# Kernel tuning notes

Measured on AMD Instinct MI355X. Metric: run time of the kernel, lower is better.

## Reference

```python
import jax, jax.numpy as jnp
import numpy as np

B, N, C = 16, 4096, 91            # images, proposals/image, classes (incl. background)
H, W = 800.0, 1333.0              # image shape
SCORE_THRESH = 0.05
NMS_THRESH = 0.5
K = 100                           # detections_per_img (greedy NMS steps)
M = 4096                          # top-M candidate prefilter before NMS
OFFSET = 1.0e4                    # class offset for batched NMS (>> max coord)
DW_CLAMP = float(np.log(1000.0 / 16.0))


def setup_inputs():
    key = jax.random.key(0)
    k1, k2, k3, k4, k5, k6 = jax.random.split(key, 6)
    class_logits = jax.random.normal(k1, (B * N, C), jnp.float32) * 2.0
    box_regression = jax.random.normal(k2, (B * N, C * 4), jnp.float32) * 0.1
    # valid proposal boxes (x1 < x2, y1 < y2, inside image)
    x1 = jax.random.uniform(k3, (B, N, 1)) * (W - 64.0)
    y1 = jax.random.uniform(k4, (B, N, 1)) * (H - 64.0)
    bw = jax.random.uniform(k5, (B, N, 1)) * 256.0 + 16.0
    bh = jax.random.uniform(k6, (B, N, 1)) * 256.0 + 16.0
    proposals = jnp.concatenate([x1, y1, jnp.minimum(x1 + bw, W), jnp.minimum(y1 + bh, H)], -1)
    return {"class_logits": class_logits, "box_regression": box_regression, "proposals": proposals}


def _decode_and_clip(rel, props):
    w = props[..., 2] - props[..., 0]
    h = props[..., 3] - props[..., 1]
    cx = props[..., 0] + 0.5 * w
    cy = props[..., 1] + 0.5 * h
    dx = rel[..., 0] / 10.0
    dy = rel[..., 1] / 10.0
    dw = jnp.minimum(rel[..., 2] / 5.0, DW_CLAMP)
    dh = jnp.minimum(rel[..., 3] / 5.0, DW_CLAMP)
    pcx = dx * w[..., None] + cx[..., None]
    pcy = dy * h[..., None] + cy[..., None]
    pw = jnp.exp(dw) * w[..., None]
    ph = jnp.exp(dh) * h[..., None]
    boxes = jnp.stack([
        jnp.clip(pcx - 0.5 * pw, 0.0, W),
        jnp.clip(pcy - 0.5 * ph, 0.0, H),
        jnp.clip(pcx + 0.5 * pw, 0.0, W),
        jnp.clip(pcy + 0.5 * ph, 0.0, H)], -1)  # [B,N,C,4]
    return boxes


def _greedy_nms(boxes, scores):
    # boxes: [M,4] (already class-offset), scores: [M] (suppressed entries == -1)
    x1, y1, x2, y2 = boxes[:, 0], boxes[:, 1], boxes[:, 2], boxes[:, 3]
    area = (x2 - x1) * (y2 - y1)

    def step(sc, _):
        i = jnp.argmax(sc)
        s = sc[i]
        valid = s > 0.0
        iw = jnp.clip(jnp.minimum(x2, x2[i]) - jnp.maximum(x1, x1[i]), 0.0)
        ih = jnp.clip(jnp.minimum(y2, y2[i]) - jnp.maximum(y1, y1[i]), 0.0)
        inter = iw * ih
        iou = inter / (area + area[i] - inter + 1e-9)
        sc = jnp.where((iou > NMS_THRESH) & valid, -1.0, sc)
        sc = sc.at[i].set(-1.0)
        return sc, (i, s, valid)

    _, (idx, ss, vv) = jax.lax.scan(step, scores, None, length=K)
    return idx, ss, vv


def _post_image(boxes_all, scores_all):
    # boxes_all: [N,C,4] decoded+clipped, scores_all: [N,C] softmax scores
    boxes = boxes_all[:, 1:, :].reshape(-1, 4)          # drop background class 0
    scores = scores_all[:, 1:].reshape(-1)              # [N*(C-1)], class fastest
    labels = jnp.tile(jnp.arange(1, C, dtype=jnp.int32), N)
    scores = jnp.where(scores > SCORE_THRESH, scores, -1.0)
    top_s, top_i = jax.lax.top_k(scores, M)
    b = boxes[top_i]
    l = labels[top_i]
    ob = b + (l.astype(jnp.float32) * OFFSET)[:, None]  # batched_nms class-offset trick
    idx, ss, vv = _greedy_nms(ob, top_s)
    out_boxes = jnp.where(vv[:, None], b[idx], 0.0)     # [K,4]
    out_scores = jnp.where(vv, ss, 0.0)                 # [K]
    out_labels = jnp.where(vv, l[idx], -1)              # [K]
    return out_boxes, out_scores, out_labels, vv


def reference(class_logits, box_regression, proposals):
    pred_scores = jax.nn.softmax(class_logits, -1).reshape(B, N, C)
    rel = box_regression.reshape(B, N, C, 4)
    pred_boxes = _decode_and_clip(rel, proposals)
    boxes, scores, labels, valid = jax.vmap(_post_image)(pred_boxes, pred_scores)
    return boxes, scores, labels, valid
```

## Files before the change

kernel.cpp:

```cpp
#include <hip/hip_runtime.h>

typedef unsigned long long u64;
typedef unsigned int u32;

#define BDIM 16
#define NP   4096
#define NC   91
#define NCM1 90
#define MSEL 4096
#define NSORT 1024
#define KOUT 100
#define RSLOT 19
#define CAP_D (NP * RSLOT)
#define SCORE_T 0.05f
#define NMS_T   0.5f
#define OFFSETF 10000.0f
#define DW_CLAMP_F 4.135166556742356f
#define WF 1333.0f
#define HF 800.0f
#define GTMIN 384
#define HCAP 4096
#define FKEY (((u64)0x3E800000u) << 32)

#define TN 1024
#define RPB 64

#define DECODE_BODY(kvar, bvar, BOXDST, PACKDST)                                   \
    {                                                                              \
        int flat = (int)(~(u32)(kvar));                                            \
        int nidx = flat / NCM1;                                                    \
        int c    = flat - nidx * NCM1 + 1;                                         \
        const float* pr = props + ((long)(bvar) * NP + nidx) * 4;                  \
        float x1 = pr[0], y1 = pr[1], x2 = pr[2], y2 = pr[3];                      \
        float w = x2 - x1, h = y2 - y1;                                            \
        float cx = x1 + 0.5f * w, cy = y1 + 0.5f * h;                              \
        const float* rr = boxreg + (((long)(bvar) * NP + nidx) * NC + c) * 4;      \
        float dx = rr[0] / 10.0f, dy = rr[1] / 10.0f;                              \
        float dw = fminf(rr[2] / 5.0f, DW_CLAMP_F);                                \
        float dh = fminf(rr[3] / 5.0f, DW_CLAMP_F);                                \
        float pcx = __fadd_rn(__fmul_rn(dx, w), cx);                               \
        float pcy = __fadd_rn(__fmul_rn(dy, h), cy);                               \
        float pw  = __fmul_rn(expf(dw), w);                                        \
        float ph2 = __fmul_rn(expf(dh), h);                                        \
        float bx1 = fminf(fmaxf(pcx - 0.5f * pw, 0.0f), WF);                       \
        float by1 = fminf(fmaxf(pcy - 0.5f * ph2, 0.0f), HF);                      \
        float bx2 = fminf(fmaxf(pcx + 0.5f * pw, 0.0f), WF);                       \
        float by2 = fminf(fmaxf(pcy + 0.5f * ph2, 0.0f), HF);                      \
        BOXDST = make_float4(bx1, by1, bx2, by2);                                  \
        float offB = (float)c * OFFSETF;                                           \
        float ox1 = bx1 + offB, oy1 = by1 + offB;                                  \
        float ox2 = bx2 + offB, oy2 = by2 + offB;                                  \
        PACKDST = make_float2((ox2 - ox1) * (oy2 - oy1), (float)c);                \
    }

__global__ __launch_bounds__(1024) void k_zero(int* __restrict__ gcount,
                                               int* __restrict__ hcnt,
                                               int* __restrict__ ghist) {
    int blk = blockIdx.x;
    if (blk == 0) {
        if (threadIdx.x < BDIM) gcount[threadIdx.x] = 0;
        if (threadIdx.x >= 64 && threadIdx.x < 64 + BDIM) hcnt[threadIdx.x - 64] = 0;
    } else {
        int* g = ghist + (blk - 1) * 2048;
        for (int i = threadIdx.x; i < 2048; i += 1024) g[i] = 0;
    }
}

__global__ __launch_bounds__(256) void k_soft(const float* __restrict__ logits,
                                              u64* __restrict__ dense,
                                              int* __restrict__ gcount,
                                              u64* __restrict__ hot,
                                              int* __restrict__ hcnt,
                                              int* __restrict__ ghist) {
    __shared__ u64 stage[RPB * RSLOT];
    __shared__ u64 hstage[256];
    __shared__ int lhist[2048];
    __shared__ int s_cnt, s_base, s_hcnt, s_hbase;

    int blk  = blockIdx.x;
    int b    = blk >> 6;
    int lane = threadIdx.x & 63;
    int wid  = threadIdx.x >> 6;

    if (threadIdx.x == 0) { s_cnt = 0; s_hcnt = 0; }
    for (int i = threadIdx.x; i < 2048; i += 256) lhist[i] = 0;
    __syncthreads();

    u64 lm = (1ull << lane) - 1ull;
    for (int it = 0; it < RPB / 4; ++it) {
        int row = blk * RPB + it * 4 + wid;
        const float* lg = logits + (long)row * NC;

        float v0 = lg[lane];
        float v1 = (lane < NC - 64) ? lg[64 + lane] : -3.0e38f;
        float mx = fmaxf(v0, v1);
#pragma unroll
        for (int s = 32; s; s >>= 1) mx = fmaxf(mx, __shfl_xor(mx, s));
        float e0 = expf(v0 - mx);
        float e1 = (lane < NC - 64) ? expf(v1 - mx) : 0.0f;
        float sum = e0 + e1;
#pragma unroll
        for (int s = 32; s; s >>= 1) sum += __shfl_xor(sum, s);

        float s0 = e0 / sum;
        float s1 = e1 / sum;

        int n = row & (NP - 1);
        bool p0 = (lane >= 1) && (s0 > SCORE_T);
        bool p1 = (lane < NC - 64) && (s1 > SCORE_T);
        u64 key0 = ((u64)__float_as_uint(s0) << 32) | (u32)(~(u32)(n * NCM1 + (lane - 1)));
        u64 key1 = ((u64)__float_as_uint(s1) << 32) | (u32)(~(u32)(n * NCM1 + (64 + lane - 1)));
        u64 m0 = __ballot(p0);
        u64 m1 = __ballot(p1);
        int c0  = __popcll(m0);
        int cnt = c0 + __popcll(m1);

        int base = 0;
        if (lane == 0 && cnt) base = atomicAdd(&s_cnt, cnt);
        base = __shfl(base, 0);
        if (p0) {
            stage[base + __popcll(m0 & lm)] = key0;
            atomicAdd(&lhist[(int)(key0 >> 53)], 1);
        }
        if (p1) {
            stage[base + c0 + __popcll(m1 & lm)] = key1;
            atomicAdd(&lhist[(int)(key1 >> 53)], 1);
        }

        bool q0 = p0 && (s0 >= 0.25f);
        bool q1 = p1 && (s1 >= 0.25f);
        u64 h0 = __ballot(q0);
        u64 h1 = __ballot(q1);
        int hc0 = __popcll(h0);
        int hrow = hc0 + __popcll(h1);
        int hb = 0;
        if (lane == 0 && hrow) hb = atomicAdd(&s_hcnt, hrow);
        hb = __shfl(hb, 0);
        if (q0) hstage[hb + __popcll(h0 & lm)] = key0;
        if (q1) hstage[hb + hc0 + __popcll(h1 & lm)] = key1;
    }
    __syncthreads();

    if (threadIdx.x == 0) {
        s_base  = atomicAdd(&gcount[b], s_cnt);
        s_hbase = atomicAdd(&hcnt[b], s_hcnt);
    }
    __syncthreads();
    int m = s_cnt, base = s_base;
    u64* kb = dense + (long)b * CAP_D + base;
    for (int i = threadIdx.x; i < m; i += 256) kb[i] = stage[i];
    int hm = s_hcnt, hb2 = s_hbase;
    u64* hbp = hot + (long)b * HCAP;
    for (int i = threadIdx.x; i < hm; i += 256) {
        int pos = hb2 + i;
        if (pos < HCAP) hbp[pos] = hstage[i];
    }
    for (int i = threadIdx.x; i < 2048; i += 256) {
        int v = lhist[i];
        if (v) atomicAdd(&ghist[b * 2048 + i], v);
    }
}

__device__ __forceinline__ u64 radix_rank(const u64* __restrict__ kb, int n, int rank,
                                          int* hist, int* p_sel, int* p_gt, int tid) {
    u64 prefix = 0, mask = 0;
    const int shifts[6] = {53, 42, 31, 20, 10, 0};
    const int bitsv [6] = {11, 11, 11, 11, 10, 10};

    for (int pass = 0; pass < 6; ++pass) {
        int shift = shifts[pass];
        int nb = 1 << bitsv[pass];
        if (tid < nb) hist[tid] = 0;
        if (tid + 1024 < nb) hist[tid + 1024] = 0;
        __syncthreads();
        for (int i = tid; i < n; i += 1024) {
            u64 k = kb[i];
            if ((k & mask) == prefix)
                atomicAdd(&hist[(int)((k >> shift) & (u64)(nb - 1))], 1);
        }
        __syncthreads();
        for (int d = 1; d < nb; d <<= 1) {
            int v0 = 0, v1 = 0;
            if (tid < nb && tid + d < nb) v0 = hist[tid + d];
            if (tid + 1024 < nb && tid + 1024 + d < nb) v1 = hist[tid + 1024 + d];
            __syncthreads();
            if (tid < nb) hist[tid] += v0;
            if (tid + 1024 < nb) hist[tid + 1024] += v1;
            __syncthreads();
        }
        for (int j = tid; j < nb; j += 1024) {
            int c  = hist[j];
            int cn = (j + 1 < nb) ? hist[j + 1] : 0;
            if (c >= rank && cn < rank) { *p_sel = j; *p_gt = cn; }
        }
        __syncthreads();
        prefix |= ((u64)(*p_sel)) << shift;
        mask   |= ((u64)(nb - 1)) << shift;
        rank   -= *p_gt;
        __syncthreads();
    }
    return prefix;
}

__device__ __forceinline__ u64 radix_upper(const u64* __restrict__ kb, int n, int rank,
                                           int* hist, int* p_sel, int* p_gt, int tid) {
    int rank0 = rank;
    u64 prefix = 0, mask = 0;
    const int shifts[6] = {53, 42, 31, 20, 10, 0};
    const int bitsv [6] = {11, 11, 11, 11, 10, 10};

    for (int pass = 0; pass < 6; ++pass) {
        int shift = shifts[pass];
        int nb = 1 << bitsv[pass];
        if (tid < nb) hist[tid] = 0;
        if (tid + 1024 < nb) hist[tid + 1024] = 0;
        __syncthreads();
        for (int i = tid; i < n; i += 1024) {
            u64 k = kb[i];
            if ((k & mask) == prefix)
                atomicAdd(&hist[(int)((k >> shift) & (u64)(nb - 1))], 1);
        }
        __syncthreads();
        for (int d = 1; d < nb; d <<= 1) {
            int v0 = 0, v1 = 0;
            if (tid < nb && tid + d < nb) v0 = hist[tid + d];
            if (tid + 1024 < nb && tid + 1024 + d < nb) v1 = hist[tid + 1024 + d];
            __syncthreads();
            if (tid < nb) hist[tid] += v0;
            if (tid + 1024 < nb) hist[tid + 1024] += v1;
            __syncthreads();
        }
        for (int j = tid; j < nb; j += 1024) {
            int c  = hist[j];
            int cn = (j + 1 < nb) ? hist[j + 1] : 0;
            if (c >= rank && cn < rank) { *p_sel = j; *p_gt = cn; }
        }
        __syncthreads();
        int sel = *p_sel, gt = *p_gt;
        rank -= gt;
        __syncthreads();
        if (pass < 5) {
            if (rank0 - rank >= GTMIN)
                return prefix + ((u64)(sel + 1) << shift);
            prefix |= ((u64)sel) << shift;
            mask   |= ((u64)(nb - 1)) << shift;
        } else {
            prefix |= ((u64)sel) << shift;
        }
    }
    return prefix;
}

__global__ __launch_bounds__(TN) void k_post(const u64* __restrict__ dense,
                                             const int* __restrict__ gcount,
                                             const u64* __restrict__ hot,
                                             const int* __restrict__ hcnt,
                                             const int* __restrict__ ghist,
                                             const float* __restrict__ boxreg,
                                             const float* __restrict__ props,
                                             float* __restrict__ out) {
    __shared__ __align__(16) char ldsbuf[131072];
    __shared__ int s_cnt, s_nacc, s_sel, s_gt, s_found;

    float4* sbox  = (float4*)ldsbuf;
    float2* spack = (float2*)(ldsbuf + 16384);
    u64*    skey  = (u64*)(ldsbuf + 24576);
    int*    hist  = (int*)(ldsbuf + 32768);

    int b = blockIdx.x, tid = threadIdx.x;
    int lane = tid & 63, wid = tid >> 6;
    int n = gcount[b]; if (n > CAP_D) n = CAP_D;
    const u64* kb = dense + (long)b * CAP_D;
    u64 lm = (1ull << lane) - 1ull;
    int npad = (n + TN - 1) & ~(TN - 1);

    u64 Bthr = 0ull;
    bool hist_ok = false;
    if (n > NSORT) {
        if (tid == 0) s_found = 0;
        __syncthreads();
        if (wid == 0) {
            int c = ghist[b * 2048 + 511 - lane];
            int cum = c;
#pragma unroll
            for (int s = 1; s < 64; s <<= 1) { int o = __shfl_up(cum, s); if (lane >= s) cum += o; }
            bool hit = (cum >= NSORT);
            u64 hm = __ballot(hit);
            if (hm) {
                int l0 = __builtin_ctzll(hm);
                if (lane == l0) { s_sel = 511 - l0; s_gt = cum - c; s_found = 1; }
            }
        }
        __syncthreads();
        if (s_found && s_gt >= GTMIN) { Bthr = ((u64)(s_sel + 1)) << 53; hist_ok = true; }
        else                          Bthr = radix_upper(kb, n, NSORT, hist, &s_sel, &s_gt, tid);
    }
    int hn = hcnt[b];
    bool use_hot = hist_ok && (Bthr >= FKEY) && (hn <= HCAP);

    skey[tid] = 0ull;
    if (tid == 0) s_cnt = 0;
    __syncthreads();
    if (use_hot) {
        const u64* hb = hot + (long)b * HCAP;
        int hpad = (hn + TN - 1) & ~(TN - 1);
        for (int i0 = tid; i0 < hpad; i0 += TN) {
            bool inb = (i0 < hn);
            u64 k = inb ? hb[i0] : 0ull;
            bool pred = inb && (k >= Bthr);
            u64 mb_ = __ballot(pred);
            int cnt = __popcll(mb_);
            int bp = 0;
            if (lane == 0 && cnt) bp = atomicAdd(&s_cnt, cnt);
            bp = __shfl(bp, 0);
            if (pred) {
                int pos = bp + __popcll(mb_ & lm);
                if (pos < NSORT) skey[pos] = k;
            }
        }
    } else {
        for (int i0 = tid; i0 < npad; i0 += TN) {
            bool inb = (i0 < n);
            u64 k = inb ? kb[i0] : 0ull;
            bool pred = inb && (k >= Bthr);
            u64 mb_ = __ballot(pred);
            int cnt = __popcll(mb_);
            int bp = 0;
            if (lane == 0 && cnt) bp = atomicAdd(&s_cnt, cnt);
            bp = __shfl(bp, 0);
            if (pred) {
                int pos = bp + __popcll(mb_ & lm);
                if (pos < NSORT) skey[pos] = k;
            }
        }
    }
    __syncthreads();
    if (s_cnt > NSORT) {
        Bthr = radix_upper(kb, n, NSORT, hist, &s_sel, &s_gt, tid);
        skey[tid] = 0ull;
        if (tid == 0) s_cnt = 0;
        __syncthreads();
        for (int i0 = tid; i0 < npad; i0 += TN) {
            bool inb = (i0 < n);
            u64 k = inb ? kb[i0] : 0ull;
            bool pred = inb && (k >= Bthr);
            u64 mb_ = __ballot(pred);
            int cnt = __popcll(mb_);
            int bp = 0;
            if (lane == 0 && cnt) bp = atomicAdd(&s_cnt, cnt);
            bp = __shfl(bp, 0);
            if (pred) {
                int pos = bp + __popcll(mb_ & lm);
                if (pos < NSORT) skey[pos] = k;
            }
        }
        __syncthreads();
    }
    int mb = s_cnt; if (mb > NSORT) mb = NSORT;

    {
        u64 r = skey[tid];
        for (int kk = 2; kk <= NSORT; kk <<= 1) {
            for (int j = kk >> 1; j; j >>= 1) {
                u64 p;
                if (j >= 64) {
                    skey[tid] = r;
                    __syncthreads();
                    p = skey[tid ^ j];
                    __syncthreads();
                } else {
                    p = __shfl_xor(r, j);
                }
                bool lower = (tid & j) == 0;
                bool desc  = ((tid & kk) == 0);
                u64 mx = (r > p) ? r : p;
                u64 mn = (r > p) ? p : r;
                r = (lower == desc) ? mx : mn;
            }
        }
        skey[tid] = r;
        __syncthreads();
    }

    for (int i = tid; i < mb; i += TN) {
        u64 k = skey[i];
        float4 bx; float2 pk;
        DECODE_BODY(k, b, bx, pk);
        sbox[i] = bx;
        spack[i] = pk;
    }
    __syncthreads();

    float ax1_0 = 0, ay1_0 = 0, ax2_0 = 0, ay2_0 = 0, aar_0 = 0;
    float ax1_1 = 0, ay1_1 = 0, ax2_1 = 0, ay2_1 = 0, aar_1 = 0;
    int alb_0 = -1, alb_1 = -1;
    u64 aky_0 = 0, aky_1 = 0;
    int nacc = 0;

    if (wid == 0) {
        float4 Bv = sbox[0];
        float2 pk = spack[0];
        u64    ck = skey[0];
        for (int i = 0; i < mb && nacc < KOUT; ++i) {
            int ip = (i + 1 < mb) ? i + 1 : i;
            float4 nBv = sbox[ip];
            float2 npk = spack[ip];
            u64    nck = skey[ip];

            float areaB = pk.x;
            float labf  = pk.y;
            float off   = __fmul_rn(labf, OFFSETF);
            bool conf = false;
            if (lane < nacc && (float)alb_0 == labf) {
                float op1x = __fadd_rn(fminf(ax2_0, Bv.z), off);
                float op2x = __fadd_rn(fmaxf(ax1_0, Bv.x), off);
                float iw = fmaxf(op1x - op2x, 0.0f);
                float op1y = __fadd_rn(fminf(ay2_0, Bv.w), off);
                float op2y = __fadd_rn(fmaxf(ay1_0, Bv.y), off);
                float ih = fmaxf(op1y - op2y, 0.0f);
                float inter = iw * ih;
                float denom = areaB + aar_0 - inter + 1e-9f;
                if (inter / denom > NMS_T) conf = true;
            }
            if (64 + lane < nacc && (float)alb_1 == labf) {
                float op1x = __fadd_rn(fminf(ax2_1, Bv.z), off);
                float op2x = __fadd_rn(fmaxf(ax1_1, Bv.x), off);
                float iw = fmaxf(op1x - op2x, 0.0f);
                float op1y = __fadd_rn(fminf(ay2_1, Bv.w), off);
                float op2y = __fadd_rn(fmaxf(ay1_1, Bv.y), off);
                float ih = fmaxf(op1y - op2y, 0.0f);
                float inter = iw * ih;
                float denom = areaB + aar_1 - inter + 1e-9f;
                if (inter / denom > NMS_T) conf = true;
            }
            if (__ballot(conf) == 0ull) {
                if (nacc < 64) {
                    if (lane == nacc) {
                        ax1_0 = Bv.x; ay1_0 = Bv.y; ax2_0 = Bv.z; ay2_0 = Bv.w;
                        aar_0 = areaB; alb_0 = (int)labf; aky_0 = ck;
                    }
                } else {
                    if (lane == nacc - 64) {
                        ax1_1 = Bv.x; ay1_1 = Bv.y; ax2_1 = Bv.z; ay2_1 = Bv.w;
                        aar_1 = areaB; alb_1 = (int)labf; aky_1 = ck;
                    }
                }
                ++nacc;
            }
            Bv = nBv; pk = npk; ck = nck;
        }
        if (lane == 0) s_nacc = nacc;
    }
    __syncthreads();

    if (s_nacc < KOUT && Bthr != 0ull) {
        u64 T = 0ull;
        if (n > MSEL) T = radix_rank(kb, n, MSEL, hist, &s_sel, &s_gt, tid);

        u64*    fkey  = (u64*)ldsbuf;
        float4* fbox  = (float4*)(ldsbuf + 32768);
        float2* fpack = (float2*)(ldsbuf + 98304);

        for (int i = tid; i < MSEL; i += TN) fkey[i] = 0ull;
        if (tid == 0) s_cnt = 0;
        __syncthreads();
        for (int i0 = tid; i0 < npad; i0 += TN) {
            bool inb = (i0 < n);
            u64 k = inb ? kb[i0] : 0ull;
            bool pred = inb && (k >= T && k < Bthr);
            u64 mb_ = __ballot(pred);
            int cnt = __popcll(mb_);
            int bp = 0;
            if (lane == 0 && cnt) bp = atomicAdd(&s_cnt, cnt);
            bp = __shfl(bp, 0);
            if (pred) {
                int pos = bp + __popcll(mb_ & lm);
                if (pos < MSEL) fkey[pos] = k;
            }
        }
        __syncthreads();
        int mb2 = s_cnt; if (mb2 > MSEL) mb2 = MSEL;

        for (int kk = 2; kk <= MSEL; kk <<= 1) {
            for (int j = kk >> 1; j > 0; j >>= 1) {
                for (int t = tid; t < MSEL; t += TN) {
                    int l = t ^ j;
                    if (l > t) {
                        u64 a = fkey[t], c = fkey[l];
                        bool up = ((t & kk) == 0);
                        bool sw = up ? (a < c) : (a > c);
                        if (sw) { fkey[t] = c; fkey[l] = a; }
                    }
                }
                __syncthreads();
            }
        }

        for (int i = tid; i < mb2; i += TN) {
            u64 k = fkey[i];
            float4 bx; float2 pk;
            DECODE_BODY(k, b, bx, pk);
            fbox[i] = bx;
            fpack[i] = pk;
        }
        __syncthreads();

        if (wid == 0) {
            nacc = s_nacc;
            float4 Bv = fbox[0];
            float2 pk = fpack[0];
            u64    ck = fkey[0];
            for (int i = 0; i < mb2 && nacc < KOUT; ++i) {
                int ip = (i + 1 < mb2) ? i + 1 : i;
                float4 nBv = fbox[ip];
                float2 npk = fpack[ip];
                u64    nck = fkey[ip];

                float areaB = pk.x;
                float labf  = pk.y;
                float off   = __fmul_rn(labf, OFFSETF);
                bool conf = false;
                if (lane < nacc && (float)alb_0 == labf) {
                    float op1x = __fadd_rn(fminf(ax2_0, Bv.z), off);
                    float op2x = __fadd_rn(fmaxf(ax1_0, Bv.x), off);
                    float iw = fmaxf(op1x - op2x, 0.0f);
                    float op1y = __fadd_rn(fminf(ay2_0, Bv.w), off);
                    float op2y = __fadd_rn(fmaxf(ay1_0, Bv.y), off);
                    float ih = fmaxf(op1y - op2y, 0.0f);
                    float inter = iw * ih;
                    float denom = areaB + aar_0 - inter + 1e-9f;
                    if (inter / denom > NMS_T) conf = true;
                }
                if (64 + lane < nacc && (float)alb_1 == labf) {
                    float op1x = __fadd_rn(fminf(ax2_1, Bv.z), off);
                    float op2x = __fadd_rn(fmaxf(ax1_1, Bv.x), off);
                    float iw = fmaxf(op1x - op2x, 0.0f);
                    float op1y = __fadd_rn(fminf(ay2_1, Bv.w), off);
                    float op2y = __fadd_rn(fmaxf(ay1_1, Bv.y), off);
                    float ih = fmaxf(op1y - op2y, 0.0f);
                    float inter = iw * ih;
                    float denom = areaB + aar_1 - inter + 1e-9f;
                    if (inter / denom > NMS_T) conf = true;
                }
                if (__ballot(conf) == 0ull) {
                    if (nacc < 64) {
                        if (lane == nacc) {
                            ax1_0 = Bv.x; ay1_0 = Bv.y; ax2_0 = Bv.z; ay2_0 = Bv.w;
                            aar_0 = areaB; alb_0 = (int)labf; aky_0 = ck;
                        }
                    } else {
                        if (lane == nacc - 64) {
                            ax1_1 = Bv.x; ay1_1 = Bv.y; ax2_1 = Bv.z; ay2_1 = Bv.w;
                            aar_1 = areaB; alb_1 = (int)labf; aky_1 = ck;
                        }
                    }
                    ++nacc;
                }
                Bv = nBv; pk = npk; ck = nck;
            }
            if (lane == 0) s_nacc = nacc;
        }
        __syncthreads();
    }

    int na = s_nacc; if (na > KOUT) na = KOUT;
    if (wid == 0) {
        if (lane < na) {
            int a = lane;
            float* ob = out + ((long)b * KOUT + a) * 4;
            ob[0] = ax1_0; ob[1] = ay1_0; ob[2] = ax2_0; ob[3] = ay2_0;
            out[BDIM * KOUT * 4 + b * KOUT + a] = __uint_as_float((u32)(aky_0 >> 32));
            out[BDIM * KOUT * 5 + b * KOUT + a] = (float)alb_0;
            out[BDIM * KOUT * 6 + b * KOUT + a] = 1.0f;
        }
        if (64 + lane < na) {
            int a = 64 + lane;
            float* ob = out + ((long)b * KOUT + a) * 4;
            ob[0] = ax1_1; ob[1] = ay1_1; ob[2] = ax2_1; ob[3] = ay2_1;
            out[BDIM * KOUT * 4 + b * KOUT + a] = __uint_as_float((u32)(aky_1 >> 32));
            out[BDIM * KOUT * 5 + b * KOUT + a] = (float)alb_1;
            out[BDIM * KOUT * 6 + b * KOUT + a] = 1.0f;
        }
    }
    for (int a = tid; a < KOUT; a += TN) {
        if (a >= na) {
            float* ob = out + ((long)b * KOUT + a) * 4;
            ob[0] = 0.0f; ob[1] = 0.0f; ob[2] = 0.0f; ob[3] = 0.0f;
            out[BDIM * KOUT * 4 + b * KOUT + a] = 0.0f;
            out[BDIM * KOUT * 5 + b * KOUT + a] = -1.0f;
            out[BDIM * KOUT * 6 + b * KOUT + a] = 0.0f;
        }
    }
}

extern "C" void kernel_launch(void* const* d_in, const int* in_sizes, int n_in,
                              void* d_out, int out_size, void* d_ws, size_t ws_size,
                              hipStream_t stream) {
    const float* logits = (const float*)d_in[0];
    const float* boxreg = (const float*)d_in[1];
    const float* props  = (const float*)d_in[2];
    float* out = (float*)d_out;

    char* ws = (char*)d_ws;
    int* gcount = (int*)(ws + 0);
    int* hcnt   = (int*)(ws + 256);
    int* ghist  = (int*)(ws + 1024);
    u64* hot    = (u64*)(ws + 132096);
    u64* dense  = (u64*)(ws + 1048576);

    k_zero<<<17, 1024, 0, stream>>>(gcount, hcnt, ghist);
    k_soft<<<(BDIM * NP) / RPB, 256, 0, stream>>>(logits, dense, gcount, hot, hcnt, ghist);
    k_post<<<BDIM, TN, 0, stream>>>(dense, gcount, hot, hcnt, ghist, boxreg, props, out);
}
```

Before: 77.34 us.

## Split post-processing into prep, parallel decode and NMS walk kernels; shrink histogram

The single per-image post kernel becomes three kernels. k_prep selects and sorts the candidate keys into workspace, k_dec decodes boxes across a wider grid, and k_walk reloads the results into LDS and runs the greedy NMS. Separately, the score histogram drops from 2048 bins to 64 bins offset by HBASE, since only exponents above the score threshold occur; this cuts zeroing and global atomic work. In exchange the change adds two kernel launches and a global-memory round trip for keys, boxes and packed areas.

```diff
diff --git a/kernel.cpp b/kernel.cpp
--- a/kernel.cpp
+++ b/kernel.cpp
@@ -21,6 +21,7 @@
 #define GTMIN 384
 #define HCAP 4096
 #define FKEY (((u64)0x3E800000u) << 32)
+#define HBASE 448
 
 #define TN 1024
 #define RPB 64
@@ -56,14 +57,10 @@
 __global__ __launch_bounds__(1024) void k_zero(int* __restrict__ gcount,
                                                int* __restrict__ hcnt,
                                                int* __restrict__ ghist) {
-    int blk = blockIdx.x;
-    if (blk == 0) {
-        if (threadIdx.x < BDIM) gcount[threadIdx.x] = 0;
-        if (threadIdx.x >= 64 && threadIdx.x < 64 + BDIM) hcnt[threadIdx.x - 64] = 0;
-    } else {
-        int* g = ghist + (blk - 1) * 2048;
-        for (int i = threadIdx.x; i < 2048; i += 1024) g[i] = 0;
-    }
+    int t = threadIdx.x;
+    if (t < BDIM) gcount[t] = 0;
+    if (t >= 64 && t < 64 + BDIM) hcnt[t - 64] = 0;
+    ghist[t] = 0;
 }
 
 __global__ __launch_bounds__(256) void k_soft(const float* __restrict__ logits,
@@ -74,7 +71,7 @@
                                               int* __restrict__ ghist) {
     __shared__ u64 stage[RPB * RSLOT];
     __shared__ u64 hstage[256];
-    __shared__ int lhist[2048];
+    __shared__ int lhist[64];
     __shared__ int s_cnt, s_base, s_hcnt, s_hbase;
 
     int blk  = blockIdx.x;
@@ -83,7 +80,7 @@
     int wid  = threadIdx.x >> 6;
 
     if (threadIdx.x == 0) { s_cnt = 0; s_hcnt = 0; }
-    for (int i = threadIdx.x; i < 2048; i += 256) lhist[i] = 0;
+    if (threadIdx.x < 64) lhist[threadIdx.x] = 0;
     __syncthreads();
 
     u64 lm = (1ull << lane) - 1ull;
@@ -120,11 +117,11 @@
         base = __shfl(base, 0);
         if (p0) {
             stage[base + __popcll(m0 & lm)] = key0;
-            atomicAdd(&lhist[(int)(key0 >> 53)], 1);
+            atomicAdd(&lhist[(int)(key0 >> 53) - HBASE], 1);
         }
         if (p1) {
             stage[base + c0 + __popcll(m1 & lm)] = key1;
-            atomicAdd(&lhist[(int)(key1 >> 53)], 1);
+            atomicAdd(&lhist[(int)(key1 >> 53) - HBASE], 1);
         }
 
         bool q0 = p0 && (s0 >= 0.25f);
@@ -155,9 +152,9 @@
         int pos = hb2 + i;
         if (pos < HCAP) hbp[pos] = hstage[i];
     }
-    for (int i = threadIdx.x; i < 2048; i += 256) {
-        int v = lhist[i];
-        if (v) atomicAdd(&ghist[b * 2048 + i], v);
+    if (threadIdx.x < 64) {
+        int v = lhist[threadIdx.x];
+        if (v) atomicAdd(&ghist[b * 64 + threadIdx.x], v);
     }
 }
 
@@ -251,21 +248,17 @@
     return prefix;
 }
 
-__global__ __launch_bounds__(TN) void k_post(const u64* __restrict__ dense,
+__global__ __launch_bounds__(TN) void k_prep(const u64* __restrict__ dense,
                                              const int* __restrict__ gcount,
                                              const u64* __restrict__ hot,
                                              const int* __restrict__ hcnt,
                                              const int* __restrict__ ghist,
-                                             const float* __restrict__ boxreg,
-                                             const float* __restrict__ props,
-                                             float* __restrict__ out) {
-    __shared__ __align__(16) char ldsbuf[131072];
-    __shared__ int s_cnt, s_nacc, s_sel, s_gt, s_found;
-
-    float4* sbox  = (float4*)ldsbuf;
-    float2* spack = (float2*)(ldsbuf + 16384);
-    u64*    skey  = (u64*)(ldsbuf + 24576);
-    int*    hist  = (int*)(ldsbuf + 32768);
+                                             u64* __restrict__ sk_ws,
+                                             int* __restrict__ mb_ws,
+                                             u64* __restrict__ bthr_ws) {
+    __shared__ u64 skey[NSORT];
+    __shared__ int hist[2048];
+    __shared__ int s_cnt, s_sel, s_gt, s_found;
 
     int b = blockIdx.x, tid = threadIdx.x;
     int lane = tid & 63, wid = tid >> 6;
@@ -280,7 +273,7 @@
         if (tid == 0) s_found = 0;
         __syncthreads();
         if (wid == 0) {
-            int c = ghist[b * 2048 + 511 - lane];
+            int c = ghist[b * 64 + 63 - lane];
             int cum = c;
 #pragma unroll
             for (int s = 1; s < 64; s <<= 1) { int o = __shfl_up(cum, s); if (lane >= s) cum += o; }
@@ -378,17 +371,57 @@
                 r = (lower == desc) ? mx : mn;
             }
         }
-        skey[tid] = r;
-        __syncthreads();
-    }
-
-    for (int i = tid; i < mb; i += TN) {
-        u64 k = skey[i];
-        float4 bx; float2 pk;
-        DECODE_BODY(k, b, bx, pk);
-        sbox[i] = bx;
-        spack[i] = pk;
-    }
+        sk_ws[b * NSORT + tid] = r;
+    }
+    if (tid == 0) { mb_ws[b] = mb; bthr_ws[b] = Bthr; }
+}
+
+__global__ __launch_bounds__(256) void k_dec(const u64* __restrict__ sk_ws,
+                                             const int* __restrict__ mb_ws,
+                                             const float* __restrict__ boxreg,
+                                             const float* __restrict__ props,
+                                             float4* __restrict__ box_ws,
+                                             float2* __restrict__ pack_ws) {
+    int b = blockIdx.y;
+    int i = blockIdx.x * 256 + threadIdx.x;
+    if (i >= mb_ws[b]) return;
+    u64 k = sk_ws[b * NSORT + i];
+    float4 bx; float2 pk;
+    DECODE_BODY(k, b, bx, pk);
+    box_ws[b * NSORT + i] = bx;
+    pack_ws[b * NSORT + i] = pk;
+}
+
+__global__ __launch_bounds__(TN) void k_walk(const u64* __restrict__ dense,
+                                             const int* __restrict__ gcount,
+                                             const u64* __restrict__ sk_ws,
+                                             const int* __restrict__ mb_ws,
+                                             const u64* __restrict__ bthr_ws,
+                                             const float4* __restrict__ box_ws,
+                                             const float2* __restrict__ pack_ws,
+                                             const float* __restrict__ boxreg,
+                                             const float* __restrict__ props,
+                                             float* __restrict__ out) {
+    __shared__ __align__(16) char ldsbuf[131072];
+    __shared__ int s_cnt, s_nacc, s_sel, s_gt;
+
+    float4* sbox  = (float4*)ldsbuf;
+    float2* spack = (float2*)(ldsbuf + 16384);
+    u64*    skey  = (u64*)(ldsbuf + 24576);
+    int*    hist  = (int*)(ldsbuf + 32768);
+
+    int b = blockIdx.x, tid = threadIdx.x;
+    int lane = tid & 63, wid = tid >> 6;
+    int n = gcount[b]; if (n > CAP_D) n = CAP_D;
+    u64 Bthr = bthr_ws[b];
+    const u64* kb = dense + (long)b * CAP_D;
+    u64 lm = (1ull << lane) - 1ull;
+    int npad = (n + TN - 1) & ~(TN - 1);
+    int mb = mb_ws[b];
+
+    skey[tid]  = sk_ws[b * NSORT + tid];
+    sbox[tid]  = box_ws[b * NSORT + tid];
+    spack[tid] = pack_ws[b * NSORT + tid];
     __syncthreads();
 
     float ax1_0 = 0, ay1_0 = 0, ax2_0 = 0, ay2_0 = 0, aar_0 = 0;
@@ -604,11 +637,19 @@
     char* ws = (char*)d_ws;
     int* gcount = (int*)(ws + 0);
     int* hcnt   = (int*)(ws + 256);
+    u64* bthr   = (u64*)(ws + 512);
+    int* mb_ws  = (int*)(ws + 768);
     int* ghist  = (int*)(ws + 1024);
-    u64* hot    = (u64*)(ws + 132096);
+    u64* sk_ws  = (u64*)(ws + 8192);
+    float2* pack_ws = (float2*)(ws + 139264);
+    float4* box_ws  = (float4*)(ws + 270336);
+    u64* hot    = (u64*)(ws + 528384);
     u64* dense  = (u64*)(ws + 1048576);
 
-    k_zero<<<17, 1024, 0, stream>>>(gcount, hcnt, ghist);
+    k_zero<<<1, 1024, 0, stream>>>(gcount, hcnt, ghist);
     k_soft<<<(BDIM * NP) / RPB, 256, 0, stream>>>(logits, dense, gcount, hot, hcnt, ghist);
-    k_post<<<BDIM, TN, 0, stream>>>(dense, gcount, hot, hcnt, ghist, boxreg, props, out);
-}
+    k_prep<<<BDIM, TN, 0, stream>>>(dense, gcount, hot, hcnt, ghist, sk_ws, mb_ws, bthr);
+    k_dec<<<dim3(4, BDIM), 256, 0, stream>>>(sk_ws, mb_ws, boxreg, props, box_ws, pack_ws);
+    k_walk<<<BDIM, TN, 0, stream>>>(dense, gcount, sk_ws, mb_ws, bthr,
+                                    box_ws, pack_ws, boxreg, props, out);
+}
```

New measurement: 79.02 us. 1.02x slower.
